# Performance work log

Measured on AMD Instinct MI355X. Metric: run time of the kernel, lower is better.

Reference implementation:

```python
import jax, jax.numpy as jnp
import numpy as np

EMBED_DIM = 1024
NUM_HEADS = 8
SEQ_LEN = 2048
EPS = 1e-6


def setup_inputs() -> dict:
    key = jax.random.key(0)
    ks = jax.random.split(key, 8)
    E, NH, S = EMBED_DIM, NUM_HEADS, SEQ_LEN
    q = jax.random.normal(ks[0], (S, E), jnp.float32)
    k = jax.random.normal(ks[1], (S, E), jnp.float32)
    v = jax.random.normal(ks[2], (S, E), jnp.float32)
    # gate projections: weights init'd to zeros in the module; use small random
    # values so the gate math is exercised. Biases follow the module's init.
    Wi = 0.02 * jax.random.normal(ks[3], (NH, 3 * E), jnp.float32)
    bi = jnp.linspace(3.0, 6.0, NH, dtype=jnp.float32)
    Wf = 0.02 * jax.random.normal(ks[4], (NH, 3 * E), jnp.float32)
    bf = jnp.sqrt(0.1) * jax.random.normal(ks[5], (NH,), jnp.float32)
    # ResidualLayerNorm (xLSTM-style): effective scale = 1 + weight, no bias
    ln_weight = jnp.zeros((E,), jnp.float32)
    return {"q": q, "k": k, "v": v, "Wi": Wi, "bi": bi, "Wf": Wf, "bf": bf,
            "ln_weight": ln_weight}


def _mlstm_parallel(q, k, v, Wi, bi, Wf, bf, ln_weight):
    S, E = q.shape
    NH = Wi.shape[0]
    DH = E // NH
    gate_in = jnp.concatenate((q, k, v), axis=1)            # (S, 3E)
    ig = (gate_in @ Wi.T + bi).T[:, :, None]                # (NH, S, 1)
    fg = (gate_in @ Wf.T + bf).T[:, :, None]                # (NH, S, 1)

    qh = q.reshape(S, NH, DH).transpose(1, 0, 2)            # (NH, S, DH)
    kh = k.reshape(S, NH, DH).transpose(1, 0, 2)
    vh = v.reshape(S, NH, DH).transpose(1, 0, 2)

    # cumulative log forget gates
    log_f = jax.nn.log_sigmoid(fg)                          # (NH, S, 1)
    log_f_cum = jnp.concatenate(
        [jnp.zeros((NH, 1, 1), q.dtype), jnp.cumsum(log_f, axis=1)], axis=1
    )                                                       # (NH, S+1, 1)
    log_fg_mat = log_f_cum - log_f_cum.transpose(0, 2, 1)   # (NH, S+1, S+1)
    causal = jnp.tril(jnp.ones((S, S), bool))
    log_fg_mat = jnp.where(causal, log_fg_mat[:, 1:, 1:], -jnp.inf)  # (NH,S,S)

    log_D = log_fg_mat + ig.transpose(0, 2, 1)              # (NH, S, S)
    max_log_D = jnp.max(log_D, axis=-1, keepdims=True)      # (NH, S, 1)
    D = jnp.exp(log_D - max_log_D)                          # stabilized

    qk = jnp.einsum('hsd,htd->hst', qh, kh) / jnp.sqrt(jnp.asarray(DH, q.dtype))
    C = qk * D                                              # (NH, S, S)
    normalizer = jnp.maximum(jnp.abs(jnp.sum(C, axis=-1, keepdims=True)),
                             jnp.exp(-max_log_D))
    C_norm = C / (normalizer + EPS)
    h = jnp.einsum('hst,htd->hsd', C_norm, vh)              # (NH, S, DH)
    h = h.transpose(1, 0, 2).reshape(S, E)

    # residual layer norm: LN(h) * (1 + weight), no bias
    mu = jnp.mean(h, axis=-1, keepdims=True)
    var = jnp.mean(jnp.square(h - mu), axis=-1, keepdims=True)
    h_norm = (h - mu) * jax.lax.rsqrt(var + 1e-5)
    return h_norm * (1.0 + ln_weight)


def reference(q, k, v, Wi, bi, Wf, bf, ln_weight):
    return _mlstm_parallel(q, k, v, Wi, bi, Wf, bf, ln_weight)
```

## Files before the change

kernel.cpp:

```cpp
#include <hip/hip_runtime.h>
#include <math.h>

#define S_LEN 2048
#define EMB   1024
#define NHEAD 8
#define DH    128
#define E3    3072
#define BM    32
#define NSPLIT 3
#define QSTRIDE  136
#define VTSTRIDE 40
#define PTSTRIDE 40

typedef __bf16 bf16x8 __attribute__((ext_vector_type(8)));
typedef __bf16 bf16x4 __attribute__((ext_vector_type(4)));
typedef float  f32x4  __attribute__((ext_vector_type(4)));

__global__ __launch_bounds__(256) void gates_cvt_transpose_kernel(
    const float* __restrict__ q, const float* __restrict__ k,
    const float* __restrict__ v,
    const float* __restrict__ Wi, const float* __restrict__ bi,
    const float* __restrict__ Wf, const float* __restrict__ bf,
    __bf16* __restrict__ Qh, __bf16* __restrict__ Ql,
    __bf16* __restrict__ Kh, __bf16* __restrict__ Kl,
    __bf16* __restrict__ Vt,
    float* __restrict__ ig, float* __restrict__ lf)
{
    const int tid = threadIdx.x;
    __shared__ union {
        float red[16][4];
        __bf16 tile[32][33];
    } sh;

    if (blockIdx.x < S_LEN) {
        const int t = blockIdx.x;
        const float4 qv = ((const float4*)q)[(size_t)t * 256 + tid];
        const float4 kv = ((const float4*)k)[(size_t)t * 256 + tid];
        const float4 vv = ((const float4*)v)[(size_t)t * 256 + tid];
        {
            size_t idx = (size_t)t * 256 + tid;
            bf16x4 hi, lo;
            hi[0]=(__bf16)qv.x; hi[1]=(__bf16)qv.y; hi[2]=(__bf16)qv.z; hi[3]=(__bf16)qv.w;
            lo[0]=(__bf16)(qv.x-(float)hi[0]); lo[1]=(__bf16)(qv.y-(float)hi[1]);
            lo[2]=(__bf16)(qv.z-(float)hi[2]); lo[3]=(__bf16)(qv.w-(float)hi[3]);
            ((bf16x4*)Qh)[idx] = hi; ((bf16x4*)Ql)[idx] = lo;
            hi[0]=(__bf16)kv.x; hi[1]=(__bf16)kv.y; hi[2]=(__bf16)kv.z; hi[3]=(__bf16)kv.w;
            lo[0]=(__bf16)(kv.x-(float)hi[0]); lo[1]=(__bf16)(kv.y-(float)hi[1]);
            lo[2]=(__bf16)(kv.z-(float)hi[2]); lo[3]=(__bf16)(kv.w-(float)hi[3]);
            ((bf16x4*)Kh)[idx] = hi; ((bf16x4*)Kl)[idx] = lo;
        }
        float acc[16];
        #pragma unroll
        for (int g = 0; g < 16; ++g) {
            const float4* w4 = (const float4*)((g < 8) ? (Wi + g * E3) : (Wf + (g - 8) * E3));
            float4 a = w4[tid], b = w4[256 + tid], c = w4[512 + tid];
            acc[g] = a.x*qv.x + a.y*qv.y + a.z*qv.z + a.w*qv.w
                   + b.x*kv.x + b.y*kv.y + b.z*kv.z + b.w*kv.w
                   + c.x*vv.x + c.y*vv.y + c.z*vv.z + c.w*vv.w;
        }
        const int w = tid >> 6, lane = tid & 63;
        #pragma unroll
        for (int g = 0; g < 16; ++g) {
            float x = acc[g];
            for (int o = 32; o > 0; o >>= 1) x += __shfl_down(x, o, 64);
            if (lane == 0) sh.red[g][w] = x;
        }
        __syncthreads();
        if (tid < 16) {
            float s = sh.red[tid][0] + sh.red[tid][1] + sh.red[tid][2] + sh.red[tid][3];
            if (tid < 8) {
                ig[tid * S_LEN + t] = s + bi[tid];
            } else {
                int h = tid - 8;
                float x = s + bf[h];
                lf[h * S_LEN + t] = fminf(x, 0.f) - log1pf(expf(-fabsf(x)));
            }
        }
    } else {
        const int tb = blockIdx.x - S_LEN;
        const int sb = (tb & 63) * 32, eb = (tb >> 6) * 32;
        #pragma unroll
        for (int i = 0; i < 4; ++i) {
            int lin = tid + i * 256;
            int sr = lin >> 5, ec = lin & 31;
            sh.tile[ec][sr] = (__bf16)v[(size_t)(sb + sr) * EMB + eb + ec];
        }
        __syncthreads();
        #pragma unroll
        for (int i = 0; i < 4; ++i) {
            int lin = tid + i * 256;
            int er = lin >> 5, sc = lin & 31;
            Vt[(size_t)(eb + er) * S_LEN + sb + sc] = sh.tile[er][sc];
        }
    }
}

__global__ __launch_bounds__(256) void cumsum_aux_kernel(
    const float* __restrict__ lf, const float* __restrict__ ig,
    float* __restrict__ F, float* __restrict__ ug,
    float* __restrict__ umax, float* __restrict__ upmax)
{
    const int h = blockIdx.x, tid = threadIdx.x;
    __shared__ float ssum[256];
    __shared__ float morig[256];
    float loc[8];
    const int base = tid * 8;
    float s = 0.f;
    for (int i = 0; i < 8; i++) { s += lf[h * S_LEN + base + i]; loc[i] = s; }
    ssum[tid] = s;
    __syncthreads();
    for (int o = 1; o < 256; o <<= 1) {
        float add = (tid >= o) ? ssum[tid - o] : 0.f;
        __syncthreads();
        ssum[tid] += add;
        __syncthreads();
    }
    float prev = (tid > 0) ? ssum[tid - 1] : 0.f;
    float* Fh = F + h * (S_LEN + 1);
    if (tid == 0) Fh[0] = 0.f;
    float Fv[8];
    for (int i = 0; i < 8; i++) { Fv[i] = prev + loc[i]; Fh[base + i + 1] = Fv[i]; }

    const float* igh = ig + h * S_LEN;
    float pm[8];
    float runm = -INFINITY;
    #pragma unroll
    for (int i = 0; i < 8; i++) {
        float u = igh[base + i] - Fv[i];
        ug[h * S_LEN + base + i] = u;
        runm = fmaxf(runm, u);
        pm[i] = runm;
    }
    morig[tid] = runm;
    __syncthreads();
    const int g0 = tid & ~3;
    float pfx = -INFINITY;
    for (int j = g0; j < tid; ++j) pfx = fmaxf(pfx, morig[j]);
    #pragma unroll
    for (int i = 0; i < 8; i++)
        upmax[h * S_LEN + base + i] = fmaxf(pfx, pm[i]);
    if ((tid & 3) == 0) {
        float mm = fmaxf(fmaxf(morig[tid], morig[tid + 1]),
                         fmaxf(morig[tid + 2], morig[tid + 3]));
        umax[h * 64 + (tid >> 2)] = mm;
    }
}

__global__ __launch_bounds__(256, 3) void mlstm_mfma(
    const __bf16* __restrict__ Qhg, const __bf16* __restrict__ Qlg,
    const __bf16* __restrict__ Khg, const __bf16* __restrict__ Klg,
    const __bf16* __restrict__ Vtg,
    const float* __restrict__ ug, const float* __restrict__ umaxg,
    const float* __restrict__ upmaxg, const float* __restrict__ F,
    __bf16* __restrict__ Opart, float* __restrict__ msplit,
    float* __restrict__ lsplit)
{
    const int flat = blockIdx.x;
    const int h = flat & 7;
    const int rest = flat >> 3;
    const int xx = rest & 31, z = rest >> 5;
    const int tid  = threadIdx.x;
    const int lane = tid & 63, w = tid >> 6;
    const int quad = lane >> 4, l15 = lane & 15;
    const int mi = w & 1, ni = w >> 1;

    __shared__ __bf16 Qh[BM * QSTRIDE], Ql[BM * QSTRIDE];
    __shared__ __bf16 Kh[BM * QSTRIDE], Kl[BM * QSTRIDE];
    __shared__ __bf16 Vt[DH * VTSTRIDE];
    __shared__ __bf16 Pt[BM * PTSTRIDE];
    __shared__ float tsum[2][BM];

    const float* Fh = F + h * (S_LEN + 1);
    const float* ugh = ug + h * S_LEN;
    const float scale = 0.088388347648318447f;
    const int kr  = tid >> 4, kc8 = tid & 15;
    const int vr0 = tid >> 2, vc0 = tid & 3;

    for (int pair = 0; pair < 2; ++pair) {
        const int qt = (pair == 0) ? xx : 63 - xx;
        const int qb = qt * BM;
        const int nj = qt + 1;
        const int j0 = (z * nj) / NSPLIT, j1 = ((z + 1) * nj) / NSPLIT;

        __syncthreads();
        #pragma unroll
        for (int i = 0; i < 2; ++i) {
            int row = kr + 16 * i;
            size_t g = (size_t)(qb + row) * EMB + h * DH + kc8 * 8;
            *(bf16x8*)&Qh[row * QSTRIDE + kc8 * 8] = *(const bf16x8*)(Qhg + g);
            *(bf16x8*)&Ql[row * QSTRIDE + kc8 * 8] = *(const bf16x8*)(Qlg + g);
        }
        float fq[4], dm[4];
        #pragma unroll
        for (int r = 0; r < 4; ++r) {
            int ri = mi * 16 + quad * 4 + r;
            fq[r] = Fh[qb + ri + 1];
            dm[r] = upmaxg[h * S_LEN + qb + ri];
        }
        float m_r[4] = {-INFINITY, -INFINITY, -INFINITY, -INFINITY};
        float l_r[4] = {0.f, 0.f, 0.f, 0.f};
        f32x4 Oacc[4] = {{0,0,0,0},{0,0,0,0},{0,0,0,0},{0,0,0,0}};

        bf16x8 pk[2], pl[2], pv[2];
        if (j0 < j1) {
            const int tb = j0 * BM;
            #pragma unroll
            for (int i = 0; i < 2; ++i) {
                int row = kr + 16 * i;
                size_t g = (size_t)(tb + row) * EMB + h * DH + kc8 * 8;
                pk[i] = *(const bf16x8*)(Khg + g);
                pl[i] = *(const bf16x8*)(Klg + g);
                pv[i] = *(const bf16x8*)(Vtg + (size_t)(h * DH + vr0 + 64 * i) * S_LEN + tb + vc0 * 8);
            }
        }

        for (int j = j0; j < j1; ++j) {
            const int tb = j * BM;
            const bool diag = (j == qt);
            __syncthreads();
            #pragma unroll
            for (int i = 0; i < 2; ++i) {
                int row = kr + 16 * i;
                *(bf16x8*)&Kh[row * QSTRIDE + kc8 * 8] = pk[i];
                *(bf16x8*)&Kl[row * QSTRIDE + kc8 * 8] = pl[i];
                *(bf16x8*)&Vt[(vr0 + 64 * i) * VTSTRIDE + vc0 * 8] = pv[i];
            }
            __syncthreads();
            if (j + 1 < j1) {
                const int tb2 = tb + BM;
                #pragma unroll
                for (int i = 0; i < 2; ++i) {
                    int row = kr + 16 * i;
                    size_t g = (size_t)(tb2 + row) * EMB + h * DH + kc8 * 8;
                    pk[i] = *(const bf16x8*)(Khg + g);
                    pl[i] = *(const bf16x8*)(Klg + g);
                    pv[i] = *(const bf16x8*)(Vtg + (size_t)(h * DH + vr0 + 64 * i) * S_LEN + tb2 + vc0 * 8);
                }
            }
            f32x4 Sacc = {0, 0, 0, 0};
            #pragma unroll
            for (int kk = 0; kk < 4; ++kk) {
                const int ao = (mi * 16 + l15) * QSTRIDE + kk * 32 + quad * 8;
                const int bo = (ni * 16 + l15) * QSTRIDE + kk * 32 + quad * 8;
                bf16x8 ah = *(const bf16x8*)&Qh[ao];
                bf16x8 al = *(const bf16x8*)&Ql[ao];
                bf16x8 bh = *(const bf16x8*)&Kh[bo];
                bf16x8 bl = *(const bf16x8*)&Kl[bo];
                Sacc = __builtin_amdgcn_mfma_f32_16x16x32_bf16(ah, bh, Sacc, 0, 0, 0);
                Sacc = __builtin_amdgcn_mfma_f32_16x16x32_bf16(ah, bl, Sacc, 0, 0, 0);
                Sacc = __builtin_amdgcn_mfma_f32_16x16x32_bf16(al, bh, Sacc, 0, 0, 0);
            }
            const int tc = ni * 16 + l15;
            const float ut = ugh[tb + tc];
            const float umj = umaxg[h * 64 + j];
            #pragma unroll
            for (int r = 0; r < 4; ++r) {
                int ri = mi * 16 + quad * 4 + r;
                float mt = fq[r] + (diag ? dm[r] : umj);
                float mn = fmaxf(m_r[r], mt);
                float alpha = __expf(m_r[r] - mn);
                m_r[r] = mn;
                l_r[r] *= alpha;
                Oacc[0][r] *= alpha; Oacc[1][r] *= alpha;
                Oacc[2][r] *= alpha; Oacc[3][r] *= alpha;
                float p = __expf(fq[r] + ut - mn) * Sacc[r] * scale;
                if (diag && (tc > ri)) p = 0.f;
                float x = p;
                #pragma unroll
                for (int o = 1; o < 16; o <<= 1) x += __shfl_xor(x, o);
                if (l15 == 0) tsum[ni][ri] = x;
                Pt[ri * PTSTRIDE + tc] = (__bf16)p;
            }
            __syncthreads();
            #pragma unroll
            for (int r = 0; r < 4; ++r) {
                int ri = mi * 16 + quad * 4 + r;
                l_r[r] += tsum[0][ri] + tsum[1][ri];
            }
            bf16x8 pa = *(const bf16x8*)&Pt[(mi * 16 + l15) * PTSTRIDE + quad * 8];
            #pragma unroll
            for (int nt = 0; nt < 4; ++nt) {
                int n = ni * 64 + nt * 16 + l15;
                bf16x4 lo = *(const bf16x4*)&Vt[n * VTSTRIDE + quad * 8];
                bf16x4 hi = *(const bf16x4*)&Vt[n * VTSTRIDE + quad * 8 + 4];
                bf16x8 b;
                b[0] = lo[0]; b[1] = lo[1]; b[2] = lo[2]; b[3] = lo[3];
                b[4] = hi[0]; b[5] = hi[1]; b[6] = hi[2]; b[7] = hi[3];
                Oacc[nt] = __builtin_amdgcn_mfma_f32_16x16x32_bf16(pa, b, Oacc[nt], 0, 0, 0);
            }
        }
        __bf16* Oz = Opart + (size_t)z * S_LEN * EMB;
        #pragma unroll
        for (int nt = 0; nt < 4; ++nt) {
            #pragma unroll
            for (int r = 0; r < 4; ++r) {
                int ri = mi * 16 + quad * 4 + r;
                Oz[(size_t)(qb + ri) * EMB + h * DH + ni * 64 + nt * 16 + l15] =
                    (__bf16)Oacc[nt][r];
            }
        }
        if (ni == 0 && l15 == 0) {
            #pragma unroll
            for (int r = 0; r < 4; ++r) {
                int ri = mi * 16 + quad * 4 + r;
                msplit[(z * NHEAD + h) * S_LEN + qb + ri] = m_r[r];
                lsplit[(z * NHEAD + h) * S_LEN + qb + ri] = l_r[r];
            }
        }
    }
}

__global__ __launch_bounds__(256) void combine_ln_kernel(
    const __bf16* __restrict__ Opart, const float* __restrict__ msplit,
    const float* __restrict__ lsplit, const float* __restrict__ lnw,
    float* __restrict__ out)
{
    const int s = blockIdx.x, tid = threadIdx.x;
    __shared__ float es_s[NSPLIT][NHEAD];
    __shared__ float rn_s[NHEAD];
    __shared__ float red[4];
    if (tid < NHEAD) {
        float mz[NSPLIT], lz[NSPLIT];
        float m = -INFINITY;
        #pragma unroll
        for (int zz = 0; zz < NSPLIT; ++zz) {
            mz[zz] = msplit[(zz * NHEAD + tid) * S_LEN + s];
            lz[zz] = lsplit[(zz * NHEAD + tid) * S_LEN + s];
            m = fmaxf(m, mz[zz]);
        }
        float l = 0.f;
        #pragma unroll
        for (int zz = 0; zz < NSPLIT; ++zz) {
            float e = __expf(mz[zz] - m);
            es_s[zz][tid] = e;
            l += e * lz[zz];
        }
        rn_s[tid] = 1.f / (fmaxf(fabsf(l), __expf(-m)) + 1e-6f);
    }
    __syncthreads();
    const size_t SE = (size_t)S_LEN * EMB;
    float x[4];
    float sum = 0.f;
    #pragma unroll
    for (int i = 0; i < 4; i++) {
        int col = tid + i * 256;
        int hh = col >> 7;
        size_t off = (size_t)s * EMB + col;
        float val = 0.f;
        #pragma unroll
        for (int zz = 0; zz < NSPLIT; ++zz)
            val += es_s[zz][hh] * (float)Opart[zz * SE + off];
        x[i] = val * rn_s[hh];
        sum += x[i];
    }
    for (int o = 32; o > 0; o >>= 1) sum += __shfl_down(sum, o, 64);
    if ((tid & 63) == 0) red[tid >> 6] = sum;
    __syncthreads();
    sum = red[0] + red[1] + red[2] + red[3];
    const float mu = sum * (1.f / EMB);
    float vs = 0.f;
    #pragma unroll
    for (int i = 0; i < 4; i++) { float d = x[i] - mu; vs += d * d; }
    __syncthreads();
    for (int o = 32; o > 0; o >>= 1) vs += __shfl_down(vs, o, 64);
    if ((tid & 63) == 0) red[tid >> 6] = vs;
    __syncthreads();
    vs = red[0] + red[1] + red[2] + red[3];
    const float rstd = rsqrtf(vs * (1.f / EMB) + 1e-5f);
    #pragma unroll
    for (int i = 0; i < 4; i++) {
        int c = tid + i * 256;
        out[(size_t)s * EMB + c] = (x[i] - mu) * rstd * (1.f + lnw[c]);
    }
}

extern "C" void kernel_launch(void* const* d_in, const int* in_sizes, int n_in,
                              void* d_out, int out_size, void* d_ws, size_t ws_size,
                              hipStream_t stream)
{
    const float* q   = (const float*)d_in[0];
    const float* k   = (const float*)d_in[1];
    const float* v   = (const float*)d_in[2];
    const float* Wi  = (const float*)d_in[3];
    const float* bi  = (const float*)d_in[4];
    const float* Wf  = (const float*)d_in[5];
    const float* bf  = (const float*)d_in[6];
    const float* lnw = (const float*)d_in[7];
    float* out = (float*)d_out;

    float* ws = (float*)d_ws;
    float* ig    = ws;
    float* lf    = ig + NHEAD * S_LEN;
    float* F     = lf + NHEAD * S_LEN;
    float* ugw   = F + NHEAD * (S_LEN + 1);
    float* umaxw = ugw + NHEAD * S_LEN;
    float* upmaxw= umaxw + NHEAD * 64;
    __bf16* Qh = (__bf16*)(upmaxw + NHEAD * S_LEN);
    const size_t SEb = (size_t)S_LEN * EMB;
    __bf16* Ql  = Qh + SEb;
    __bf16* Kh  = Ql + SEb;
    __bf16* Kl  = Kh + SEb;
    __bf16* Vtg = Kl + SEb;
    __bf16* Opart = Vtg + SEb;
    float* msplit = (float*)(Opart + (size_t)NSPLIT * SEb);
    float* lsplit = msplit + NSPLIT * NHEAD * S_LEN;

    gates_cvt_transpose_kernel<<<2 * S_LEN, 256, 0, stream>>>(
        q, k, v, Wi, bi, Wf, bf, Qh, Ql, Kh, Kl, Vtg, ig, lf);
    cumsum_aux_kernel<<<NHEAD, 256, 0, stream>>>(lf, ig, F, ugw, umaxw, upmaxw);
    mlstm_mfma<<<32 * NHEAD * NSPLIT, 256, 0, stream>>>(
        Qh, Ql, Kh, Kl, Vtg, ugw, umaxw, upmaxw, F, Opart, msplit, lsplit);
    combine_ln_kernel<<<S_LEN, 256, 0, stream>>>(Opart, msplit, lsplit, lnw, out);
}
```

Measured before the change: 181.6 us.

## Restructure mLSTM attention to 64-row query tiles with per-wave rows and register Q

The attention kernel changes from 32x32 tiles split across a 2x2 wave grid to 64-row query tiles, where each wave owns 16 query rows and the full 32-column key tile. Per-wave row ownership drops the shared tsum reduction and one block barrier per key tile, and P is now written to a per-wave LDS slice. The Q split is now read from global memory into registers on every key-tile iteration instead of staged once in LDS. The split count goes from 3 to 4, launch bounds drop to 2 blocks per CU, and -INFINITY is replaced by -1e30 so masked rows avoid NaN. The trade is more accumulator registers and repeated Q loads in exchange for fewer barriers and more K/V reuse per block.

```diff
diff --git a/kernel.cpp b/kernel.cpp
--- a/kernel.cpp
+++ b/kernel.cpp
@@ -6,9 +6,10 @@
 #define NHEAD 8
 #define DH    128
 #define E3    3072
-#define BM    32
-#define NSPLIT 3
-#define QSTRIDE  136
+#define BM    64
+#define BN    32
+#define NSPLIT 4
+#define KSTRIDE  136
 #define VTSTRIDE 40
 #define PTSTRIDE 40
 
@@ -123,7 +124,7 @@
 
     const float* igh = ig + h * S_LEN;
     float pm[8];
-    float runm = -INFINITY;
+    float runm = -1e30f;
     #pragma unroll
     for (int i = 0; i < 8; i++) {
         float u = igh[base + i] - Fv[i];
@@ -134,7 +135,7 @@
     morig[tid] = runm;
     __syncthreads();
     const int g0 = tid & ~3;
-    float pfx = -INFINITY;
+    float pfx = -1e30f;
     for (int j = g0; j < tid; ++j) pfx = fmaxf(pfx, morig[j]);
     #pragma unroll
     for (int i = 0; i < 8; i++)
@@ -146,7 +147,7 @@
     }
 }
 
-__global__ __launch_bounds__(256, 3) void mlstm_mfma(
+__global__ __launch_bounds__(256, 2) void mlstm_mfma(
     const __bf16* __restrict__ Qhg, const __bf16* __restrict__ Qlg,
     const __bf16* __restrict__ Khg, const __bf16* __restrict__ Klg,
     const __bf16* __restrict__ Vtg,
@@ -158,52 +159,44 @@
     const int flat = blockIdx.x;
     const int h = flat & 7;
     const int rest = flat >> 3;
-    const int xx = rest & 31, z = rest >> 5;
+    const int xx = rest & 15, z = rest >> 4;
     const int tid  = threadIdx.x;
     const int lane = tid & 63, w = tid >> 6;
     const int quad = lane >> 4, l15 = lane & 15;
-    const int mi = w & 1, ni = w >> 1;
-
-    __shared__ __bf16 Qh[BM * QSTRIDE], Ql[BM * QSTRIDE];
-    __shared__ __bf16 Kh[BM * QSTRIDE], Kl[BM * QSTRIDE];
+
+    __shared__ __bf16 Kh[BN * KSTRIDE], Kl[BN * KSTRIDE];
     __shared__ __bf16 Vt[DH * VTSTRIDE];
-    __shared__ __bf16 Pt[BM * PTSTRIDE];
-    __shared__ float tsum[2][BM];
-
-    const float* Fh = F + h * (S_LEN + 1);
+    __shared__ __bf16 Pt[4][16 * PTSTRIDE];
+
+    const float* Fh  = F  + h * (S_LEN + 1);
     const float* ugh = ug + h * S_LEN;
     const float scale = 0.088388347648318447f;
     const int kr  = tid >> 4, kc8 = tid & 15;
     const int vr0 = tid >> 2, vc0 = tid & 3;
 
     for (int pair = 0; pair < 2; ++pair) {
-        const int qt = (pair == 0) ? xx : 63 - xx;
+        const int qt = (pair == 0) ? xx : 31 - xx;
         const int qb = qt * BM;
-        const int nj = qt + 1;
+        const int nj = 2 * qt + 2;
         const int j0 = (z * nj) / NSPLIT, j1 = ((z + 1) * nj) / NSPLIT;
 
-        __syncthreads();
-        #pragma unroll
-        for (int i = 0; i < 2; ++i) {
-            int row = kr + 16 * i;
-            size_t g = (size_t)(qb + row) * EMB + h * DH + kc8 * 8;
-            *(bf16x8*)&Qh[row * QSTRIDE + kc8 * 8] = *(const bf16x8*)(Qhg + g);
-            *(bf16x8*)&Ql[row * QSTRIDE + kc8 * 8] = *(const bf16x8*)(Qlg + g);
-        }
-        float fq[4], dm[4];
+        float fq[4], upm[4];
+        int sglob[4], sblk[4];
         #pragma unroll
         for (int r = 0; r < 4; ++r) {
-            int ri = mi * 16 + quad * 4 + r;
-            fq[r] = Fh[qb + ri + 1];
-            dm[r] = upmaxg[h * S_LEN + qb + ri];
-        }
-        float m_r[4] = {-INFINITY, -INFINITY, -INFINITY, -INFINITY};
+            int s = qb + w * 16 + quad * 4 + r;
+            sglob[r] = s; sblk[r] = s >> 5;
+            fq[r]  = Fh[s + 1];
+            upm[r] = upmaxg[h * S_LEN + s];
+        }
+        float m_r[4] = {-1e30f, -1e30f, -1e30f, -1e30f};
         float l_r[4] = {0.f, 0.f, 0.f, 0.f};
-        f32x4 Oacc[4] = {{0,0,0,0},{0,0,0,0},{0,0,0,0},{0,0,0,0}};
+        f32x4 Oacc[8] = {{0,0,0,0},{0,0,0,0},{0,0,0,0},{0,0,0,0},
+                         {0,0,0,0},{0,0,0,0},{0,0,0,0},{0,0,0,0}};
 
         bf16x8 pk[2], pl[2], pv[2];
         if (j0 < j1) {
-            const int tb = j0 * BM;
+            const int tb = j0 * BN;
             #pragma unroll
             for (int i = 0; i < 2; ++i) {
                 int row = kr + 16 * i;
@@ -215,19 +208,18 @@
         }
 
         for (int j = j0; j < j1; ++j) {
-            const int tb = j * BM;
-            const bool diag = (j == qt);
+            const int tb = j * BN;
             __syncthreads();
             #pragma unroll
             for (int i = 0; i < 2; ++i) {
                 int row = kr + 16 * i;
-                *(bf16x8*)&Kh[row * QSTRIDE + kc8 * 8] = pk[i];
-                *(bf16x8*)&Kl[row * QSTRIDE + kc8 * 8] = pl[i];
+                *(bf16x8*)&Kh[row * KSTRIDE + kc8 * 8] = pk[i];
+                *(bf16x8*)&Kl[row * KSTRIDE + kc8 * 8] = pl[i];
                 *(bf16x8*)&Vt[(vr0 + 64 * i) * VTSTRIDE + vc0 * 8] = pv[i];
             }
             __syncthreads();
             if (j + 1 < j1) {
-                const int tb2 = tb + BM;
+                const int tb2 = tb + BN;
                 #pragma unroll
                 for (int i = 0; i < 2; ++i) {
                     int row = kr + 16 * i;
@@ -237,74 +229,77 @@
                     pv[i] = *(const bf16x8*)(Vtg + (size_t)(h * DH + vr0 + 64 * i) * S_LEN + tb2 + vc0 * 8);
                 }
             }
-            f32x4 Sacc = {0, 0, 0, 0};
+            bf16x8 qh[4], ql[4];
+            {
+                const size_t qrow = (size_t)(qb + w * 16 + l15) * EMB + h * DH + quad * 8;
+                #pragma unroll
+                for (int kk = 0; kk < 4; ++kk) {
+                    qh[kk] = *(const bf16x8*)(Qhg + qrow + kk * 32);
+                    ql[kk] = *(const bf16x8*)(Qlg + qrow + kk * 32);
+                }
+            }
+            f32x4 S0 = {0,0,0,0}, S1 = {0,0,0,0};
             #pragma unroll
             for (int kk = 0; kk < 4; ++kk) {
-                const int ao = (mi * 16 + l15) * QSTRIDE + kk * 32 + quad * 8;
-                const int bo = (ni * 16 + l15) * QSTRIDE + kk * 32 + quad * 8;
-                bf16x8 ah = *(const bf16x8*)&Qh[ao];
-                bf16x8 al = *(const bf16x8*)&Ql[ao];
-                bf16x8 bh = *(const bf16x8*)&Kh[bo];
-                bf16x8 bl = *(const bf16x8*)&Kl[bo];
-                Sacc = __builtin_amdgcn_mfma_f32_16x16x32_bf16(ah, bh, Sacc, 0, 0, 0);
-                Sacc = __builtin_amdgcn_mfma_f32_16x16x32_bf16(ah, bl, Sacc, 0, 0, 0);
-                Sacc = __builtin_amdgcn_mfma_f32_16x16x32_bf16(al, bh, Sacc, 0, 0, 0);
-            }
-            const int tc = ni * 16 + l15;
-            const float ut = ugh[tb + tc];
+                const int co = kk * 32 + quad * 8;
+                bf16x8 bh0 = *(const bf16x8*)&Kh[l15 * KSTRIDE + co];
+                bf16x8 bl0 = *(const bf16x8*)&Kl[l15 * KSTRIDE + co];
+                S0 = __builtin_amdgcn_mfma_f32_16x16x32_bf16(qh[kk], bh0, S0, 0, 0, 0);
+                S0 = __builtin_amdgcn_mfma_f32_16x16x32_bf16(qh[kk], bl0, S0, 0, 0, 0);
+                S0 = __builtin_amdgcn_mfma_f32_16x16x32_bf16(ql[kk], bh0, S0, 0, 0, 0);
+                bf16x8 bh1 = *(const bf16x8*)&Kh[(16 + l15) * KSTRIDE + co];
+                bf16x8 bl1 = *(const bf16x8*)&Kl[(16 + l15) * KSTRIDE + co];
+                S1 = __builtin_amdgcn_mfma_f32_16x16x32_bf16(qh[kk], bh1, S1, 0, 0, 0);
+                S1 = __builtin_amdgcn_mfma_f32_16x16x32_bf16(qh[kk], bl1, S1, 0, 0, 0);
+                S1 = __builtin_amdgcn_mfma_f32_16x16x32_bf16(ql[kk], bh1, S1, 0, 0, 0);
+            }
+            const int t0 = tb + l15, t1 = tb + 16 + l15;
+            const float ut0 = ugh[t0], ut1 = ugh[t1];
             const float umj = umaxg[h * 64 + j];
             #pragma unroll
             for (int r = 0; r < 4; ++r) {
-                int ri = mi * 16 + quad * 4 + r;
-                float mt = fq[r] + (diag ? dm[r] : umj);
+                float mt = (j < sblk[r]) ? (fq[r] + umj)
+                         : (j == sblk[r]) ? (fq[r] + upm[r]) : -1e30f;
                 float mn = fmaxf(m_r[r], mt);
                 float alpha = __expf(m_r[r] - mn);
                 m_r[r] = mn;
                 l_r[r] *= alpha;
-                Oacc[0][r] *= alpha; Oacc[1][r] *= alpha;
-                Oacc[2][r] *= alpha; Oacc[3][r] *= alpha;
-                float p = __expf(fq[r] + ut - mn) * Sacc[r] * scale;
-                if (diag && (tc > ri)) p = 0.f;
-                float x = p;
+                #pragma unroll
+                for (int nt = 0; nt < 8; ++nt) Oacc[nt][r] *= alpha;
+                float p0 = __expf(fq[r] + ut0 - mn) * S0[r] * scale;
+                float p1 = __expf(fq[r] + ut1 - mn) * S1[r] * scale;
+                if (j >= sblk[r]) {
+                    if (t0 > sglob[r]) p0 = 0.f;
+                    if (t1 > sglob[r]) p1 = 0.f;
+                }
+                float x = p0 + p1;
                 #pragma unroll
                 for (int o = 1; o < 16; o <<= 1) x += __shfl_xor(x, o);
-                if (l15 == 0) tsum[ni][ri] = x;
-                Pt[ri * PTSTRIDE + tc] = (__bf16)p;
-            }
-            __syncthreads();
+                l_r[r] += x;
+                const int prow = (quad * 4 + r) * PTSTRIDE;
+                Pt[w][prow + l15]      = (__bf16)p0;
+                Pt[w][prow + 16 + l15] = (__bf16)p1;
+            }
+            bf16x8 pa = *(const bf16x8*)&Pt[w][l15 * PTSTRIDE + quad * 8];
+            #pragma unroll
+            for (int nt = 0; nt < 8; ++nt) {
+                bf16x8 vb = *(const bf16x8*)&Vt[(nt * 16 + l15) * VTSTRIDE + quad * 8];
+                Oacc[nt] = __builtin_amdgcn_mfma_f32_16x16x32_bf16(pa, vb, Oacc[nt], 0, 0, 0);
+            }
+        }
+        __bf16* Oz = Opart + (size_t)z * S_LEN * EMB;
+        #pragma unroll
+        for (int nt = 0; nt < 8; ++nt) {
             #pragma unroll
             for (int r = 0; r < 4; ++r) {
-                int ri = mi * 16 + quad * 4 + r;
-                l_r[r] += tsum[0][ri] + tsum[1][ri];
-            }
-            bf16x8 pa = *(const bf16x8*)&Pt[(mi * 16 + l15) * PTSTRIDE + quad * 8];
-            #pragma unroll
-            for (int nt = 0; nt < 4; ++nt) {
-                int n = ni * 64 + nt * 16 + l15;
-                bf16x4 lo = *(const bf16x4*)&Vt[n * VTSTRIDE + quad * 8];
-                bf16x4 hi = *(const bf16x4*)&Vt[n * VTSTRIDE + quad * 8 + 4];
-                bf16x8 b;
-                b[0] = lo[0]; b[1] = lo[1]; b[2] = lo[2]; b[3] = lo[3];
-                b[4] = hi[0]; b[5] = hi[1]; b[6] = hi[2]; b[7] = hi[3];
-                Oacc[nt] = __builtin_amdgcn_mfma_f32_16x16x32_bf16(pa, b, Oacc[nt], 0, 0, 0);
-            }
-        }
-        __bf16* Oz = Opart + (size_t)z * S_LEN * EMB;
-        #pragma unroll
-        for (int nt = 0; nt < 4; ++nt) {
+                Oz[(size_t)sglob[r] * EMB + h * DH + nt * 16 + l15] = (__bf16)Oacc[nt][r];
+            }
+        }
+        if (l15 == 0) {
             #pragma unroll
             for (int r = 0; r < 4; ++r) {
-                int ri = mi * 16 + quad * 4 + r;
-                Oz[(size_t)(qb + ri) * EMB + h * DH + ni * 64 + nt * 16 + l15] =
-                    (__bf16)Oacc[nt][r];
-            }
-        }
-        if (ni == 0 && l15 == 0) {
-            #pragma unroll
-            for (int r = 0; r < 4; ++r) {
-                int ri = mi * 16 + quad * 4 + r;
-                msplit[(z * NHEAD + h) * S_LEN + qb + ri] = m_r[r];
-                lsplit[(z * NHEAD + h) * S_LEN + qb + ri] = l_r[r];
+                msplit[(z * NHEAD + h) * S_LEN + sglob[r]] = m_r[r];
+                lsplit[(z * NHEAD + h) * S_LEN + sglob[r]] = l_r[r];
             }
         }
     }
@@ -321,7 +316,7 @@
     __shared__ float red[4];
     if (tid < NHEAD) {
         float mz[NSPLIT], lz[NSPLIT];
-        float m = -INFINITY;
+        float m = -1e30f;
         #pragma unroll
         for (int zz = 0; zz < NSPLIT; ++zz) {
             mz[zz] = msplit[(zz * NHEAD + tid) * S_LEN + s];
@@ -408,7 +403,7 @@
     gates_cvt_transpose_kernel<<<2 * S_LEN, 256, 0, stream>>>(
         q, k, v, Wi, bi, Wf, bf, Qh, Ql, Kh, Kl, Vtg, ig, lf);
     cumsum_aux_kernel<<<NHEAD, 256, 0, stream>>>(lf, ig, F, ugw, umaxw, upmaxw);
-    mlstm_mfma<<<32 * NHEAD * NSPLIT, 256, 0, stream>>>(
+    mlstm_mfma<<<16 * NHEAD * NSPLIT, 256, 0, stream>>>(
         Qh, Ql, Kh, Kl, Vtg, ugw, umaxw, upmaxw, F, Opart, msplit, lsplit);
     combine_ln_kernel<<<S_LEN, 256, 0, stream>>>(Opart, msplit, lsplit, lnw, out);
 }
```

Result: faster. 159.9 us (-11.9%).
